# Kernel optimization log

Measured on AMD Instinct MI355X. Metric: run time of the kernel, lower is better.

Reference implementation:

```python
import jax, jax.numpy as jnp
import numpy as np

B, L = 32, 2048
AA_VOCAB, AA_EMB = 26, 5
C = 256                 # num_channels
S = 8                   # prot_section_size
GO_VOCAB, GO = 30000, 256
K = 15                  # conv kernel size


def setup_inputs() -> dict:
    key = jax.random.key(0)
    ks = jax.random.split(key, 10)
    inp = {
        "input_seq": jax.random.randint(ks[0], (B, L), 0, AA_VOCAB),
        "input_go_term": jax.random.randint(ks[1], (B,), 0, GO_VOCAB),
        "aa_emb": jax.random.normal(ks[2], (AA_VOCAB, AA_EMB), jnp.float32),
        "conv1_w": jax.random.normal(ks[3], (2 * C, AA_EMB, K), jnp.float32) * 0.05,
        "conv1_b": jnp.zeros((2 * C,), jnp.float32),
        "conv2_w": jax.random.normal(ks[4], (C, 2 * C, K), jnp.float32) * 0.02,
        "conv2_b": jnp.zeros((C,), jnp.float32),
        "go_table": jax.random.normal(ks[5], (GO_VOCAB, GO), jnp.float32),
        "attn_w": jax.random.normal(ks[6], (GO, C * S), jnp.float32) * 0.02,
        "attn_b": jnp.zeros((GO,), jnp.float32),
    }
    return inp


def reference(input_seq, input_go_term, aa_emb, conv1_w, conv1_b,
              conv2_w, conv2_b, go_table, attn_w, attn_b):
    # --- ProteinEncoder (dropout = identity at inference) ---
    x = aa_emb[input_seq]                      # [B, L, 5]
    x = jnp.transpose(x, (0, 2, 1))            # [B, 5, L]
    dn = ('NCH', 'OIH', 'NCH')
    x = jax.lax.conv_general_dilated(x, conv1_w, (1,), 'VALID', dimension_numbers=dn)
    x = jax.nn.relu(x + conv1_b[None, :, None])   # [B, 2C, L-14]
    x = jax.lax.conv_general_dilated(x, conv2_w, (1,), 'VALID', dimension_numbers=dn)
    x = jax.nn.relu(x + conv2_b[None, :, None])   # [B, C, P], P = L-28

    # --- section the protein (same row-major view as torch .view) ---
    b, c, P = x.shape
    n = P // S
    rem = P % S
    head = rem // 2
    tail = P - (rem - head)
    enc = x[:, :, head:tail].reshape(b, c * S, n)   # [B, C*S, N]

    # --- Attn('general'): score_i = go . (W @ section_i + bias), softmax over i ---
    go = go_table[input_go_term]                     # [B, G]
    proj = jnp.einsum('bpn,gp->bgn', enc, attn_w) + attn_b[:, None]  # [B, G, N]
    energies = jnp.einsum('bg,bgn->bn', go, proj)    # [B, N]
    attn = jax.nn.softmax(energies, axis=-1)         # [B, N]

    # --- context: [B,1,N] bmm [B,N,C*S] -> [B, C*S] ---
    ctx = jnp.einsum('bn,bpn->bp', attn, enc)
    return ctx
```

## Files before the change

### kernel.cpp

```cpp
#include <hip/hip_runtime.h>

#define B_ 32
#define L_ 2048
#define C1 512
#define C2 256
#define KW 15
#define P1 2034
#define NJ 2016
#define NSEC 252
#define GOD 256

typedef _Float16 f16;
typedef __attribute__((ext_vector_type(4))) _Float16 f16x4;
typedef __attribute__((ext_vector_type(8))) _Float16 f16x8;
typedef __attribute__((ext_vector_type(4))) float f32x4;

#define WS_Y1T   0ull
#define WS_W2R   66650112ull
#define WS_W1R   70582272ull
#define WS_E     70688768ull
#define WS_V     103718912ull
#define WS_EN    103981056ull

__device__ __forceinline__ void gl16(const f16* g, f16* l) {
    __builtin_amdgcn_global_load_lds((const __attribute__((address_space(1))) char*)(g),
                                     (__attribute__((address_space(3))) char*)(l), 16, 0, 0);
}

__global__ void k_prep(const float* __restrict__ w2, f16* __restrict__ w2r,
                       const float* __restrict__ w1, f16* __restrict__ w1r,
                       float* __restrict__ energies) {
    const int t0 = blockIdx.x * blockDim.x + threadIdx.x;
    const int nthr = gridDim.x * blockDim.x;
    for (int idx = t0; idx < C2 * C1 * KW; idx += nthr) {
        int o = idx / (C1 * KW);
        int rem = idx - o * (C1 * KW);
        int c = rem / KW;
        int k = rem - c * KW;
        w2r[((size_t)k * C2 + o) * C1 + c] = (f16)w2[idx];
    }
    for (int idx = t0; idx < C1 * 104; idx += nthr) {
        int o = idx / 104;
        int col = idx - o * 104;
        int e = col >> 4, k = col & 15;
        float val = (e < 5 && k < 15) ? w1[o * 75 + e * 15 + k] : 0.f;
        w1r[idx] = (f16)val;
    }
    for (int idx = t0; idx < B_ * NSEC; idx += nthr) energies[idx] = 0.f;
}

__global__ __launch_bounds__(256) void k_conv1(const int* __restrict__ seq,
                                               const float* __restrict__ aa_emb,
                                               const f16* __restrict__ w1r,
                                               const float* __restrict__ b1,
                                               f16* __restrict__ y1t) {
    __shared__ f16 Aw[256 * 104];
    __shared__ f16 Bx[64 * 104];
    __shared__ float xs[5][80];
    const int b = blockIdx.z, o0 = blockIdx.y * 256, pos0 = blockIdx.x * 64;
    const int tid = threadIdx.x;
    const int wave = tid >> 6, lane = tid & 63;
    const int lm = lane & 15, lh = lane >> 4;

#pragma unroll
    for (int r = 0; r < 13; ++r) {
        int q = r * 4096 + wave * 1024 + lane * 16;
        gl16(w1r + o0 * 104 + (q >> 1), Aw + (q >> 1));
    }
    if (tid < 79) {
        int l = pos0 + tid;
        if (l < L_) {
            int a = seq[b * L_ + l];
#pragma unroll
            for (int e = 0; e < 5; ++e) xs[e][tid] = aa_emb[a * 5 + e];
        } else {
#pragma unroll
            for (int e = 0; e < 5; ++e) xs[e][tid] = 0.f;
        }
    }
    __syncthreads();
    for (int idx = tid; idx < 64 * 104; idx += 256) {
        int j = idx / 104, col = idx - j * 104;
        int e = col >> 4, k = col & 15;
        Bx[idx] = (e < 5 && k < 15) ? (f16)xs[e][j + k] : (f16)0.f;
    }
    __syncthreads();

    f32x4 acc[4][4];
#pragma unroll
    for (int mf = 0; mf < 4; ++mf)
#pragma unroll
        for (int nf = 0; nf < 4; ++nf) acc[mf][nf] = (f32x4){0.f, 0.f, 0.f, 0.f};

    const char* Ab = (const char*)Aw + (wave * 64 + lm) * 208 + lh * 16;
    const char* Bb = (const char*)Bx + lm * 208 + lh * 16;
#pragma unroll
    for (int ks = 0; ks < 3; ++ks) {
        f16x8 av[4], bv[4];
#pragma unroll
        for (int mf = 0; mf < 4; ++mf) av[mf] = *(const f16x8*)(Ab + mf * 16 * 208 + ks * 64);
#pragma unroll
        for (int nf = 0; nf < 4; ++nf) bv[nf] = *(const f16x8*)(Bb + nf * 16 * 208 + ks * 64);
#pragma unroll
        for (int mf = 0; mf < 4; ++mf)
#pragma unroll
            for (int nf = 0; nf < 4; ++nf)
                acc[mf][nf] = __builtin_amdgcn_mfma_f32_16x16x32_f16(av[mf], bv[nf], acc[mf][nf], 0, 0, 0);
    }

#pragma unroll
    for (int nf = 0; nf < 4; ++nf) {
        int pos = pos0 + nf * 16 + lm;
        if (pos >= P1) continue;
#pragma unroll
        for (int mf = 0; mf < 4; ++mf) {
            int ob = wave * 64 + mf * 16 + lh * 4;
            f16x4 st;
#pragma unroll
            for (int r = 0; r < 4; ++r)
                st[r] = (f16)fmaxf(acc[mf][nf][r] + b1[o0 + ob + r], 0.f);
            *(f16x4*)(y1t + ((size_t)b * P1 + pos) * C1 + o0 + ob) = st;
        }
    }
}

__global__ __launch_bounds__(256, 2) void k_conv2(const f16* __restrict__ y1t,
                                                  const f16* __restrict__ w2r,
                                                  const float* __restrict__ b2,
                                                  const float* __restrict__ v,
                                                  f16* __restrict__ E,
                                                  float* __restrict__ energies) {
    __shared__ f16 As[3 * 8192];
    __shared__ f16 Bs[10240];
    const int b = blockIdx.y;
    const int n0 = blockIdx.x << 7;
    const int tid = threadIdx.x;
    const int wave = tid >> 6, lane = tid & 63;
    const int lm = lane & 15, lh = lane >> 4;
    const int wm = wave >> 1, wn = wave & 1;
    const size_t ybase = (size_t)b * P1 + n0 + 2;

    f32x4 acc[8][4];
#pragma unroll
    for (int mf = 0; mf < 8; ++mf)
#pragma unroll
        for (int nf = 0; nf < 4; ++nf) acc[mf][nf] = (f32x4){0.f, 0.f, 0.f, 0.f};

#define STAGE_A(slot, cc2, k2, h2)                                                    \
    {                                                                                 \
        _Pragma("unroll")                                                             \
        for (int rr = 0; rr < 4; ++rr) {                                              \
            int q = rr * 4096 + tid * 16;                                             \
            int row = q >> 6;                                                         \
            int sw = ((q >> 4) & 3) ^ ((row >> 1) & 3);                               \
            const f16* g = w2r + (size_t)(k2) * 131072 + row * C1 + (cc2) * 64 + (h2) * 32 + sw * 8; \
            gl16(g, As + (slot) * 8192 + (q >> 1));                                   \
        }                                                                             \
    }
#define STAGE_B(cc2)                                                                  \
    {                                                                                 \
        _Pragma("unroll")                                                             \
        for (int rr = 0; rr < 5; ++rr) {                                              \
            int q = rr * 4096 + tid * 16;                                             \
            int row = q >> 7;                                                         \
            int sw = ((q >> 4) & 7) ^ (row & 7);                                      \
            const f16* g = y1t + (ybase + row) * C1 + (cc2) * 64 + sw * 8;            \
            gl16(g, Bs + (q >> 1));                                                   \
        }                                                                             \
    }

    STAGE_B(0);
    STAGE_A(0, 0, 0, 0);
    STAGE_A(1, 0, 0, 1);
    asm volatile("s_waitcnt vmcnt(4)" ::: "memory");
    __builtin_amdgcn_s_barrier();

    const int swA = (lh ^ ((lm >> 1) & 3)) << 4;
    int sl = 0;

#pragma unroll 1
    for (int cc = 0; cc < 8; ++cc) {
#pragma unroll 1
        for (int k = 0; k < KW; ++k) {
#pragma unroll
            for (int h = 0; h < 2; ++h) {
                int k2 = k + 1, cc2 = cc;
                if (k2 == 15) { k2 = 0; cc2 = cc + 1; }
                const bool have2 = (cc2 < 8);
                const bool bnd = (k == 0 && h == 0 && cc > 0);
                const int s2 = (sl >= 1) ? sl - 1 : 2;

                if (bnd) {
                    STAGE_B(cc);
                    STAGE_A(s2, cc2, k2, h);
                    asm volatile("s_waitcnt vmcnt(4)" ::: "memory");
                    __builtin_amdgcn_s_barrier();
                }

                const char* Ab = (const char*)As + sl * 16384;
                f16x8 bv[4], av[8];
#pragma unroll
                for (int nf = 0; nf < 4; ++nf) {
                    int brow = wn * 64 + nf * 16 + lm + k;
                    bv[nf] = *(const f16x8*)((const char*)Bs + brow * 128 + ((((h << 2) | lh) ^ (brow & 7)) << 4));
                }
#pragma unroll
                for (int i = 0; i < 8; ++i)
                    av[i] = *(const f16x8*)(Ab + (wm * 128 + i * 16 + lm) * 64 + swA);
                if (!bnd && have2) STAGE_A(s2, cc2, k2, h);

                __builtin_amdgcn_s_setprio(1);
#pragma unroll
                for (int i = 0; i < 8; ++i)
#pragma unroll
                    for (int nf = 0; nf < 4; ++nf)
                        acc[i][nf] = __builtin_amdgcn_mfma_f32_16x16x32_f16(av[i], bv[nf], acc[i][nf], 0, 0, 0);
                __builtin_amdgcn_s_setprio(0);
                if (have2) { asm volatile("s_waitcnt vmcnt(4)" ::: "memory"); }
                else       { asm volatile("s_waitcnt vmcnt(0)" ::: "memory"); }
                __builtin_amdgcn_s_barrier();

                sl = (sl == 2) ? 0 : sl + 1;
            }
        }
    }

    const float* vb = v + b * 2048;
#pragma unroll
    for (int nf = 0; nf < 4; ++nf) {
        const int j = n0 + wn * 64 + nf * 16 + lm;
        if (j >= NJ) continue;
        const int jq = j / NSEC;
        const int jm = j - jq * NSEC;
        float esum = 0.f;
#pragma unroll
        for (int mf = 0; mf < 8; ++mf) {
            const int ob = wm * 128 + mf * 16 + lh * 4;
#pragma unroll
            for (int r = 0; r < 4; ++r) {
                float val = fmaxf(acc[mf][nf][r] + b2[ob + r], 0.f);
                E[((size_t)b * C2 + ob + r) * NJ + j] = (f16)val;
                esum = fmaf(val, vb[(ob + r) * 8 + jq], esum);
            }
        }
        atomicAdd(&energies[b * NSEC + jm], esum);
    }
#undef STAGE_A
#undef STAGE_B
}

__global__ void k_v(const int* __restrict__ goidx, const float* __restrict__ go_table,
                    const float* __restrict__ attn_w, float* __restrict__ v) {
    const int b = blockIdx.y;
    const int p = blockIdx.x * 256 + threadIdx.x;
    const float* go = go_table + (size_t)goidx[b] * GOD;
    float acc = 0.f;
    for (int g = 0; g < GOD; ++g) acc = fmaf(go[g], attn_w[g * 2048 + p], acc);
    v[b * 2048 + p] = acc;
}

__global__ __launch_bounds__(256) void k_ctx(const f16* __restrict__ E,
                                             const float* __restrict__ energies,
                                             float* __restrict__ out) {
    __shared__ float red[256];
    __shared__ float attn_s[NSEC];
    const int b = blockIdx.y;
    const int tid = threadIdx.x;

    float ev = 0.f, e = -1e30f;
    if (tid < NSEC) { ev = energies[b * NSEC + tid]; e = ev; }
    red[tid] = e;
    __syncthreads();
    for (int s = 128; s > 0; s >>= 1) {
        if (tid < s) red[tid] = fmaxf(red[tid], red[tid + s]);
        __syncthreads();
    }
    float m = red[0];
    __syncthreads();
    float ex = (tid < NSEC) ? __expf(ev - m) : 0.f;
    red[tid] = ex;
    __syncthreads();
    for (int s = 128; s > 0; s >>= 1) {
        if (tid < s) red[tid] += red[tid + s];
        __syncthreads();
    }
    float inv = 1.f / red[0];
    if (tid < NSEC) attn_s[tid] = ex * inv;
    __syncthreads();

    const int wave = tid >> 6, lane = tid & 63;
    const int c = blockIdx.x * 4 + wave;
    float a0 = 0.f, a1 = 0.f, a2 = 0.f, a3 = 0.f;
    if (lane < 63) {
        a0 = attn_s[lane * 4];     a1 = attn_s[lane * 4 + 1];
        a2 = attn_s[lane * 4 + 2]; a3 = attn_s[lane * 4 + 3];
    }
    const f16* Er = E + ((size_t)b * C2 + c) * NJ;
#pragma unroll
    for (int r = 0; r < 8; ++r) {
        float s = 0.f;
        if (lane < 63) {
            f16x4 ee = *(const f16x4*)(Er + r * NSEC + lane * 4);
            s = (float)ee[0] * a0 + (float)ee[1] * a1 + (float)ee[2] * a2 + (float)ee[3] * a3;
        }
#pragma unroll
        for (int off = 32; off > 0; off >>= 1) s += __shfl_down(s, off);
        if (lane == 0) out[b * 2048 + c * 8 + r] = s;
    }
}

extern "C" void kernel_launch(void* const* d_in, const int* in_sizes, int n_in,
                              void* d_out, int out_size, void* d_ws, size_t ws_size,
                              hipStream_t stream) {
    const int*   seq      = (const int*)d_in[0];
    const int*   goidx    = (const int*)d_in[1];
    const float* aa_emb   = (const float*)d_in[2];
    const float* w1       = (const float*)d_in[3];
    const float* b1       = (const float*)d_in[4];
    const float* w2       = (const float*)d_in[5];
    const float* b2       = (const float*)d_in[6];
    const float* go_table = (const float*)d_in[7];
    const float* attn_w   = (const float*)d_in[8];
    float* out = (float*)d_out;

    char* ws = (char*)d_ws;
    f16*   y1t      = (f16*)(ws + WS_Y1T);
    f16*   w2r      = (f16*)(ws + WS_W2R);
    f16*   w1r      = (f16*)(ws + WS_W1R);
    f16*   E        = (f16*)(ws + WS_E);
    float* v        = (float*)(ws + WS_V);
    float* energies = (float*)(ws + WS_EN);

    hipLaunchKernelGGL(k_prep,  dim3(512),         dim3(256), 0, stream, w2, w2r, w1, w1r, energies);
    hipLaunchKernelGGL(k_conv1, dim3(32, 2, B_),   dim3(256), 0, stream, seq, aa_emb, w1r, b1, y1t);
    hipLaunchKernelGGL(k_v,     dim3(8, B_),       dim3(256), 0, stream, goidx, go_table, attn_w, v);
    hipLaunchKernelGGL(k_conv2, dim3(16, B_),      dim3(256), 0, stream, y1t, w2r, b2, v, E, energies);
    hipLaunchKernelGGL(k_ctx,   dim3(64, B_),      dim3(256), 0, stream, E, energies, out);
}
```

Measured before the change: 272.6 us.

## Merge prep, conv1 and go-projection into one heterogeneous front kernel

```diff
diff --git a/kernel.cpp b/kernel.cpp
--- a/kernel.cpp
+++ b/kernel.cpp
@@ -17,7 +17,6 @@
 
 #define WS_Y1T   0ull
 #define WS_W2R   66650112ull
-#define WS_W1R   70582272ull
 #define WS_E     70688768ull
 #define WS_V     103718912ull
 #define WS_EN    103981056ull
@@ -27,45 +26,59 @@
                                      (__attribute__((address_space(3))) char*)(l), 16, 0, 0);
 }
 
-__global__ void k_prep(const float* __restrict__ w2, f16* __restrict__ w2r,
-                       const float* __restrict__ w1, f16* __restrict__ w1r,
-                       float* __restrict__ energies) {
-    const int t0 = blockIdx.x * blockDim.x + threadIdx.x;
-    const int nthr = gridDim.x * blockDim.x;
-    for (int idx = t0; idx < C2 * C1 * KW; idx += nthr) {
-        int o = idx / (C1 * KW);
-        int rem = idx - o * (C1 * KW);
-        int c = rem / KW;
-        int k = rem - c * KW;
-        w2r[((size_t)k * C2 + o) * C1 + c] = (f16)w2[idx];
-    }
-    for (int idx = t0; idx < C1 * 104; idx += nthr) {
-        int o = idx / 104;
-        int col = idx - o * 104;
-        int e = col >> 4, k = col & 15;
-        float val = (e < 5 && k < 15) ? w1[o * 75 + e * 15 + k] : 0.f;
-        w1r[idx] = (f16)val;
-    }
-    for (int idx = t0; idx < B_ * NSEC; idx += nthr) energies[idx] = 0.f;
-}
-
-__global__ __launch_bounds__(256) void k_conv1(const int* __restrict__ seq,
+__global__ __launch_bounds__(256) void k_front(const float* __restrict__ w2,
+                                               f16* __restrict__ w2r,
+                                               float* __restrict__ energies,
+                                               const int* __restrict__ goidx,
+                                               const float* __restrict__ go_table,
+                                               const float* __restrict__ attn_w,
+                                               float* __restrict__ v,
+                                               const int* __restrict__ seq,
                                                const float* __restrict__ aa_emb,
-                                               const f16* __restrict__ w1r,
+                                               const float* __restrict__ w1,
                                                const float* __restrict__ b1,
                                                f16* __restrict__ y1t) {
+    const int bid = blockIdx.x;
+    const int tid = threadIdx.x;
+
+    if (bid < 512) {
+        const int t0 = bid * 256 + tid;
+        const int nthr = 512 * 256;
+        for (int idx = t0; idx < C2 * C1 * KW; idx += nthr) {
+            int o = idx / (C1 * KW);
+            int rem = idx - o * (C1 * KW);
+            int c = rem / KW;
+            int k = rem - c * KW;
+            w2r[((size_t)k * C2 + o) * C1 + c] = (f16)w2[idx];
+        }
+        for (int idx = t0; idx < B_ * NSEC; idx += nthr) energies[idx] = 0.f;
+        return;
+    }
+    if (bid < 768) {
+        const int r = bid - 512;
+        const int b = r >> 3;
+        const int p = (r & 7) * 256 + tid;
+        const float* go = go_table + (size_t)goidx[b] * GOD;
+        float acc = 0.f;
+        for (int g = 0; g < GOD; ++g) acc = fmaf(go[g], attn_w[g * 2048 + p], acc);
+        v[b * 2048 + p] = acc;
+        return;
+    }
+
     __shared__ f16 Aw[256 * 104];
     __shared__ f16 Bx[64 * 104];
     __shared__ float xs[5][80];
-    const int b = blockIdx.z, o0 = blockIdx.y * 256, pos0 = blockIdx.x * 64;
-    const int tid = threadIdx.x;
+    const int r0 = bid - 768;
+    const int b = r0 >> 6, half = (r0 >> 5) & 1, chunk = r0 & 31;
+    const int o0 = half * 256, pos0 = chunk * 64;
     const int wave = tid >> 6, lane = tid & 63;
     const int lm = lane & 15, lh = lane >> 4;
 
-#pragma unroll
-    for (int r = 0; r < 13; ++r) {
-        int q = r * 4096 + wave * 1024 + lane * 16;
-        gl16(w1r + o0 * 104 + (q >> 1), Aw + (q >> 1));
+    for (int idx = tid; idx < 256 * 104; idx += 256) {
+        int o = idx / 104, col = idx - o * 104;
+        int e = col >> 4, k = col & 15;
+        float val = (e < 5 && k < 15) ? w1[(o0 + o) * 75 + e * 15 + k] : 0.f;
+        Aw[idx] = (f16)val;
     }
     if (tid < 79) {
         int l = pos0 + tid;
@@ -108,19 +121,32 @@
                 acc[mf][nf] = __builtin_amdgcn_mfma_f32_16x16x32_f16(av[mf], bv[nf], acc[mf][nf], 0, 0, 0);
     }
 
-#pragma unroll
-    for (int nf = 0; nf < 4; ++nf) {
-        int pos = pos0 + nf * 16 + lm;
-        if (pos >= P1) continue;
-#pragma unroll
-        for (int mf = 0; mf < 4; ++mf) {
-            int ob = wave * 64 + mf * 16 + lh * 4;
-            f16x4 st;
-#pragma unroll
-            for (int r = 0; r < 4; ++r)
-                st[r] = (f16)fmaxf(acc[mf][nf][r] + b1[o0 + ob + r], 0.f);
-            *(f16x4*)(y1t + ((size_t)b * P1 + pos) * C1 + o0 + ob) = st;
-        }
+    __syncthreads();
+    {
+        f16* Ot = Aw;
+#pragma unroll
+        for (int nf = 0; nf < 4; ++nf) {
+            int pos = nf * 16 + lm;
+#pragma unroll
+            for (int mf = 0; mf < 4; ++mf) {
+                int ob = wave * 64 + mf * 16 + lh * 4;
+                f16x4 st;
+#pragma unroll
+                for (int rr = 0; rr < 4; ++rr)
+                    st[rr] = (f16)fmaxf(acc[mf][nf][rr] + b1[o0 + ob + rr], 0.f);
+                *(f16x4*)(Ot + pos * 264 + ob) = st;
+            }
+        }
+    }
+    __syncthreads();
+#pragma unroll
+    for (int rr = 0; rr < 8; ++rr) {
+        int q = rr * 4096 + tid * 16;
+        int pos = q >> 9;
+        int ob = q & 511;
+        if (pos0 + pos < P1)
+            *(f16x8*)((char*)y1t + (size_t)(b * P1 + pos0 + pos) * 1024 + half * 512 + ob) =
+                *(const f16x8*)((const char*)Aw + pos * 528 + ob);
     }
 }
 
@@ -249,16 +275,6 @@
 #undef STAGE_B
 }
 
-__global__ void k_v(const int* __restrict__ goidx, const float* __restrict__ go_table,
-                    const float* __restrict__ attn_w, float* __restrict__ v) {
-    const int b = blockIdx.y;
-    const int p = blockIdx.x * 256 + threadIdx.x;
-    const float* go = go_table + (size_t)goidx[b] * GOD;
-    float acc = 0.f;
-    for (int g = 0; g < GOD; ++g) acc = fmaf(go[g], attn_w[g * 2048 + p], acc);
-    v[b * 2048 + p] = acc;
-}
-
 __global__ __launch_bounds__(256) void k_ctx(const f16* __restrict__ E,
                                              const float* __restrict__ energies,
                                              float* __restrict__ out) {
@@ -326,14 +342,13 @@
     char* ws = (char*)d_ws;
     f16*   y1t      = (f16*)(ws + WS_Y1T);
     f16*   w2r      = (f16*)(ws + WS_W2R);
-    f16*   w1r      = (f16*)(ws + WS_W1R);
     f16*   E        = (f16*)(ws + WS_E);
     float* v        = (float*)(ws + WS_V);
     float* energies = (float*)(ws + WS_EN);
 
-    hipLaunchKernelGGL(k_prep,  dim3(512),         dim3(256), 0, stream, w2, w2r, w1, w1r, energies);
-    hipLaunchKernelGGL(k_conv1, dim3(32, 2, B_),   dim3(256), 0, stream, seq, aa_emb, w1r, b1, y1t);
-    hipLaunchKernelGGL(k_v,     dim3(8, B_),       dim3(256), 0, stream, goidx, go_table, attn_w, v);
-    hipLaunchKernelGGL(k_conv2, dim3(16, B_),      dim3(256), 0, stream, y1t, w2r, b2, v, E, energies);
-    hipLaunchKernelGGL(k_ctx,   dim3(64, B_),      dim3(256), 0, stream, E, energies, out);
-}
+    hipLaunchKernelGGL(k_front, dim3(2816),     dim3(256), 0, stream,
+                       w2, w2r, energies, goidx, go_table, attn_w, v,
+                       seq, aa_emb, w1, b1, y1t);
+    hipLaunchKernelGGL(k_conv2, dim3(16, B_),   dim3(256), 0, stream, y1t, w2r, b2, v, E, energies);
+    hipLaunchKernelGGL(k_ctx,   dim3(64, B_),   dim3(256), 0, stream, E, energies, out);
+}
```

New measurement: 343.7 us. +26.1%, slower.
